# Kernel optimization log

Measured on AMD Instinct MI355X. Metric: run time of the kernel, lower is better.

Reference implementation:

```python
import jax, jax.numpy as jnp
import numpy as np

EMBED, NH, NKV, HD, FF, EPS = 2048, 16, 4, 128, 5632, 1e-5
B, S = 2, 2048

def rmsnorm(x, w):
    xf = x.astype(jnp.float32)
    n = xf * jax.lax.rsqrt(jnp.mean(xf * xf, axis=-1, keepdims=True) + EPS)
    return n.astype(x.dtype) * w

def apply_rope(x, freqs_cis):
    # x: (b, s, h, d); freqs_cis: (s, d//2, 2)
    b, s, h, d = x.shape
    xr = x.astype(jnp.float32).reshape(b, s, h, d // 2, 2)
    f = freqs_cis.reshape(1, s, 1, d // 2, 2)
    out = jnp.stack([xr[..., 0] * f[..., 0] - xr[..., 1] * f[..., 1],
                     xr[..., 1] * f[..., 0] + xr[..., 0] * f[..., 1]], axis=-1)
    return out.reshape(b, s, h, d).astype(x.dtype)

def setup_inputs() -> dict:
    key = jax.random.key(0)
    ks = jax.random.split(key, 8)
    x = jax.random.normal(ks[0], (B, S, EMBED), dtype=jnp.float32)
    attention_mask = jnp.tril(jnp.ones((S, S), dtype=jnp.int32))[None].repeat(B, axis=0)
    # RoPE cos/sin table
    inv = 1.0 / (10000.0 ** (np.arange(0, HD, 2, dtype=np.float32) / HD))
    t = np.arange(S, dtype=np.float32)[:, None] * inv[None, :]  # (S, HD//2)
    freqs_cis = jnp.asarray(np.stack([np.cos(t), np.sin(t)], axis=-1))  # (S, HD//2, 2)
    input_pos = jnp.arange(S, dtype=jnp.int32)
    sd = 0.02
    w_qkv = jax.random.normal(ks[1], ((NH + 2 * NKV) * HD, EMBED), dtype=jnp.float32) * sd
    w_fc = jax.random.normal(ks[2], (EMBED, EMBED), dtype=jnp.float32) * sd
    w1 = jax.random.normal(ks[3], (FF, EMBED), dtype=jnp.float32) * sd
    w2 = jax.random.normal(ks[4], (FF, EMBED), dtype=jnp.float32) * sd
    w3 = jax.random.normal(ks[5], (EMBED, FF), dtype=jnp.float32) * sd
    attn_norm_w = jnp.ones((EMBED,), dtype=jnp.float32)
    ff_norm_w = jnp.ones((EMBED,), dtype=jnp.float32)
    return {"x": x, "attention_mask": attention_mask, "freqs_cis": freqs_cis,
            "input_pos": input_pos, "w_qkv": w_qkv, "w_fc": w_fc,
            "w1": w1, "w2": w2, "w3": w3,
            "attn_norm_w": attn_norm_w, "ff_norm_w": ff_norm_w}

def reference(x, attention_mask, freqs_cis, input_pos, w_qkv, w_fc, w1, w2, w3, attn_norm_w, ff_norm_w):
    b, s, _ = x.shape
    n_rep = NH // NKV
    # --- attention block ---
    h = rmsnorm(x, attn_norm_w)
    qkv = h @ w_qkv.T
    q, k, v = jnp.split(qkv, [NH * HD, NH * HD + NKV * HD], axis=-1)
    q = q.reshape(b, s, NH, HD)
    k = k.reshape(b, s, NKV, HD)
    v = v.reshape(b, s, NKV, HD)
    q = apply_rope(q, freqs_cis)
    k = apply_rope(k, freqs_cis)
    q = q.transpose(0, 2, 1, 3)                       # (b, NH, s, d)
    k = jnp.repeat(k.transpose(0, 2, 1, 3), n_rep, axis=1)  # (b, NH, s, d)
    v = jnp.repeat(v.transpose(0, 2, 1, 3), n_rep, axis=1)
    scale = 1.0 / jnp.sqrt(jnp.float32(EMBED))  # NOTE: source scales by sqrt(embedding_dim)
    scores = jnp.einsum('bhqd,bhkd->bhqk', q, k) * scale
    scores = jnp.where(attention_mask[:, None] == 0, -jnp.inf, scores)
    probs = jax.nn.softmax(scores, axis=-1)
    attn = jnp.einsum('bhqk,bhkd->bhqd', probs, v)
    attn = attn.transpose(0, 2, 1, 3).reshape(b, s, EMBED) @ w_fc.T
    h = x + attn
    # --- SwiGLU FFN ---
    g = rmsnorm(h, ff_norm_w)
    ff = (jax.nn.silu(g @ w1.T) * (g @ w2.T)) @ w3.T
    return h + ff
```

## Files before the change

kernel.cpp:

```cpp
#include <hip/hip_runtime.h>
#include <cstdint>
#include <cstddef>

typedef unsigned short u16;
typedef short bf16x8 __attribute__((ext_vector_type(8)));
typedef float f32x4 __attribute__((ext_vector_type(4)));

#define AS1C(p) ((const __attribute__((address_space(1))) void*)(p))
#define AS3(p)  ((__attribute__((address_space(3))) void*)(p))
#define MFMA_BF16 __builtin_amdgcn_mfma_f32_16x16x32_bf16

__device__ __forceinline__ u16 f2bf(float f) {
    union { float f; unsigned int u; } v; v.f = f;
    unsigned int r = v.u + 0x7fffu + ((v.u >> 16) & 1u);
    return (u16)(r >> 16);
}

struct U16x4 { u16 x, y, z, w; };

__global__ __launch_bounds__(256) void cvt_kernel(const float* __restrict__ src,
                                                  u16* __restrict__ dst, int n4) {
    int i = blockIdx.x * 256 + threadIdx.x;
    if (i < n4) {
        const float4 v = ((const float4*)src)[i];
        U16x4 o; o.x = f2bf(v.x); o.y = f2bf(v.y); o.z = f2bf(v.z); o.w = f2bf(v.w);
        ((U16x4*)dst)[i] = o;
    }
}

__global__ __launch_bounds__(256) void rmsnorm_kernel(const float* __restrict__ X,
                                                      const float* __restrict__ W,
                                                      u16* __restrict__ Out) {
    const int row = blockIdx.x;
    const int t = threadIdx.x;
    const float* xr = X + (size_t)row * 2048;
    float4 a = ((const float4*)xr)[2 * t];
    float4 b = ((const float4*)xr)[2 * t + 1];
    float ss = a.x*a.x + a.y*a.y + a.z*a.z + a.w*a.w
             + b.x*b.x + b.y*b.y + b.z*b.z + b.w*b.w;
    #pragma unroll
    for (int off = 1; off < 64; off <<= 1) ss += __shfl_xor(ss, off);
    __shared__ float red[4];
    if ((t & 63) == 0) red[t >> 6] = ss;
    __syncthreads();
    float tot = red[0] + red[1] + red[2] + red[3];
    float rs = rsqrtf(tot * (1.0f / 2048.0f) + 1e-5f);
    float vals[8] = {a.x, a.y, a.z, a.w, b.x, b.y, b.z, b.w};
    const int base = t * 8;
    u16* orow = Out + (size_t)row * 2048 + base;
    #pragma unroll
    for (int j = 0; j < 8; ++j) orow[j] = f2bf(vals[j] * rs * W[base + j]);
}

__global__ __launch_bounds__(256) void rope_kernel(const float* __restrict__ qkv,
                                                   const float* __restrict__ fr,
                                                   u16* __restrict__ Qo, u16* __restrict__ Ko,
                                                   u16* __restrict__ Vo) {
    const int tok = blockIdx.x;
    const int b = tok >> 11, s = tok & 2047;
    const int t = threadIdx.x;
    const float* row = qkv + (size_t)tok * 3072;
    const float* f = fr + (size_t)s * 128;
    #pragma unroll
    for (int i = 0; i < 4; ++i) {
        int p = t + i * 256;
        int h = p >> 6, pi = p & 63;
        float x0 = row[h * 128 + pi * 2];
        float x1 = row[h * 128 + pi * 2 + 1];
        float c = f[pi * 2], sn = f[pi * 2 + 1];
        size_t ob = ((size_t)(b * 16 + h) * 2048 + s) * 128 + pi * 2;
        Qo[ob]     = f2bf(x0 * c - x1 * sn);
        Qo[ob + 1] = f2bf(x1 * c + x0 * sn);
    }
    {
        int kh = t >> 6, pi = t & 63;
        float x0 = row[2048 + kh * 128 + pi * 2];
        float x1 = row[2048 + kh * 128 + pi * 2 + 1];
        float c = f[pi * 2], sn = f[pi * 2 + 1];
        size_t ob = ((size_t)(b * 4 + kh) * 2048 + s) * 128 + pi * 2;
        Ko[ob]     = f2bf(x0 * c - x1 * sn);
        Ko[ob + 1] = f2bf(x1 * c + x0 * sn);
    }
    #pragma unroll
    for (int i = 0; i < 2; ++i) {
        int e = t + i * 256;
        int kh = e >> 7, d = e & 127;
        Vo[((size_t)(b * 4 + kh) * 128 + d) * 2048 + s] = f2bf(row[2560 + e]);
    }
}

template <bool RESID, bool DUAL>
__global__ __launch_bounds__(256, 2) void gemm_bt(
    const u16* __restrict__ A, const u16* __restrict__ B0, const u16* __restrict__ B1,
    const float* __restrict__ RES, float* __restrict__ Cf, u16* __restrict__ Cb,
    int M, int N, int K) {
    __shared__ __align__(16) u16 As[128 * 32];
    __shared__ __align__(16) u16 Bs[128 * 32];
    __shared__ __align__(16) u16 Bs2[128 * 32];
    const int w = threadIdx.x >> 6;
    const int lane = threadIdx.x & 63;
    const int bm = blockIdx.y * 128;
    const int bn = blockIdx.x * 128;
    const int wm = (w >> 1) * 64;
    const int wn = (w & 1) * 64;
    const int lr = lane & 15;
    const int kq = (lane >> 4) * 8;
    const int srow = lane >> 2;
    const int skc = (lane & 3) * 8;
    f32x4 acc[4][4];
    f32x4 acc2[4][4];
    const f32x4 z = {0.f, 0.f, 0.f, 0.f};
    #pragma unroll
    for (int i = 0; i < 4; ++i)
        #pragma unroll
        for (int j = 0; j < 4; ++j) { acc[i][j] = z; acc2[i][j] = z; }

    for (int k0 = 0; k0 < K; k0 += 32) {
        #pragma unroll
        for (int c = 0; c < 2; ++c) {
            const int chunk = 2 * w + c;
            const int r = chunk * 16 + srow;
            const int lofs = chunk * 512 + lane * 8;
            __builtin_amdgcn_global_load_lds(AS1C(A + (size_t)(bm + r) * K + k0 + skc),
                                             AS3(&As[lofs]), 16, 0, 0);
            __builtin_amdgcn_global_load_lds(AS1C(B0 + (size_t)(bn + r) * K + k0 + skc),
                                             AS3(&Bs[lofs]), 16, 0, 0);
            if constexpr (DUAL)
                __builtin_amdgcn_global_load_lds(AS1C(B1 + (size_t)(bn + r) * K + k0 + skc),
                                                 AS3(&Bs2[lofs]), 16, 0, 0);
        }
        __syncthreads();
        bf16x8 af[4], bfr[4];
        #pragma unroll
        for (int tm = 0; tm < 4; ++tm) af[tm] = *(const bf16x8*)&As[(wm + tm * 16 + lr) * 32 + kq];
        #pragma unroll
        for (int tn = 0; tn < 4; ++tn) bfr[tn] = *(const bf16x8*)&Bs[(wn + tn * 16 + lr) * 32 + kq];
        #pragma unroll
        for (int tm = 0; tm < 4; ++tm)
            #pragma unroll
            for (int tn = 0; tn < 4; ++tn)
                acc[tm][tn] = MFMA_BF16(af[tm], bfr[tn], acc[tm][tn], 0, 0, 0);
        if constexpr (DUAL) {
            #pragma unroll
            for (int tn = 0; tn < 4; ++tn) bfr[tn] = *(const bf16x8*)&Bs2[(wn + tn * 16 + lr) * 32 + kq];
            #pragma unroll
            for (int tm = 0; tm < 4; ++tm)
                #pragma unroll
                for (int tn = 0; tn < 4; ++tn)
                    acc2[tm][tn] = MFMA_BF16(af[tm], bfr[tn], acc2[tm][tn], 0, 0, 0);
        }
        __syncthreads();
    }
    #pragma unroll
    for (int tm = 0; tm < 4; ++tm) {
        const int row0 = bm + wm + tm * 16 + (lane >> 4) * 4;
        #pragma unroll
        for (int tn = 0; tn < 4; ++tn) {
            const int col = bn + wn + tn * 16 + (lane & 15);
            #pragma unroll
            for (int r = 0; r < 4; ++r) {
                const size_t idx = (size_t)(row0 + r) * N + col;
                if constexpr (DUAL) {
                    float aa = acc[tm][tn][r];
                    float bb = acc2[tm][tn][r];
                    float sg = aa / (1.0f + __expf(-aa));
                    Cb[idx] = f2bf(sg * bb);
                } else {
                    float v = acc[tm][tn][r];
                    if constexpr (RESID) v += RES[idx];
                    Cf[idx] = v;
                }
            }
        }
    }
}

__global__ __launch_bounds__(256, 2) void attn_kernel(
    const u16* __restrict__ Q, const u16* __restrict__ Kg,
    const u16* __restrict__ Vt, u16* __restrict__ O) {
    __shared__ __align__(16) u16 Ks[16 * 512];
    __shared__ __align__(16) u16 Vs[16 * 512];
    __shared__ __align__(16) u16 Ps[4][32 * 72];
    const int qt = (int)gridDim.x - 1 - (int)blockIdx.x;
    const int h = blockIdx.y, b = blockIdx.z;
    const int kvh = h >> 2;
    const int w = threadIdx.x >> 6, lane = threadIdx.x & 63;
    const int lr = lane & 15, quad = lane >> 4;
    const int q0 = qt * 128;
    const int wq = q0 + w * 32;
    const u16* kgbase = Kg + (size_t)(b * 4 + kvh) * 2048 * 128;
    const u16* vgbase = Vt + (size_t)(b * 4 + kvh) * 128 * 2048;
    bf16x8 qf[2][4];
    #pragma unroll
    for (int mt = 0; mt < 2; ++mt)
        #pragma unroll
        for (int kk = 0; kk < 4; ++kk)
            qf[mt][kk] = *(const bf16x8*)(Q + ((size_t)(b * 16 + h) * 2048 + wq + mt * 16 + lr) * 128
                                          + kk * 32 + quad * 8);
    f32x4 o[2][8];
    const f32x4 z = {0.f, 0.f, 0.f, 0.f};
    #pragma unroll
    for (int mt = 0; mt < 2; ++mt)
        #pragma unroll
        for (int dt = 0; dt < 8; ++dt) o[mt][dt] = z;
    float m_r[2][4], l_r[2][4];
    #pragma unroll
    for (int mt = 0; mt < 2; ++mt)
        #pragma unroll
        for (int r = 0; r < 4; ++r) { m_r[mt][r] = -1e30f; l_r[mt][r] = 0.f; }
    const float scale = 0.022097086912079608f;
    const float LOG2E = 1.4426950408889634f;
    const int nkt = (q0 + 128) >> 6;

    for (int kt = 0; kt < nkt; ++kt) {
        __syncthreads();
        #pragma unroll
        for (int c = 0; c < 4; ++c) {
            const int i = w * 4 + c;
            __builtin_amdgcn_global_load_lds(
                AS1C(kgbase + (size_t)(kt * 64 + lane) * 128 + i * 8),
                AS3(&Ks[i * 512 + lane * 8]), 16, 0, 0);
            __builtin_amdgcn_global_load_lds(
                AS1C(vgbase + (size_t)((i & 1) * 64 + lane) * 2048 + kt * 64 + (i >> 1) * 8),
                AS3(&Vs[i * 512 + lane * 8]), 16, 0, 0);
        }
        __syncthreads();
        if (kt * 64 <= wq + 31) {
            f32x4 s[2][4];
            #pragma unroll
            for (int mt = 0; mt < 2; ++mt)
                #pragma unroll
                for (int nt = 0; nt < 4; ++nt) s[mt][nt] = z;
            #pragma unroll
            for (int kk = 0; kk < 4; ++kk) {
                bf16x8 kf[4];
                #pragma unroll
                for (int nt = 0; nt < 4; ++nt)
                    kf[nt] = *(const bf16x8*)&Ks[(kk * 4 + quad) * 512 + (nt * 16 + lr) * 8];
                #pragma unroll
                for (int mt = 0; mt < 2; ++mt)
                    #pragma unroll
                    for (int nt = 0; nt < 4; ++nt)
                        s[mt][nt] = MFMA_BF16(qf[mt][kk], kf[nt], s[mt][nt], 0, 0, 0);
            }
            u16* pw = &Ps[w][0];
            #pragma unroll
            for (int mt = 0; mt < 2; ++mt) {
                float mx[4];
                #pragma unroll
                for (int r = 0; r < 4; ++r) {
                    const int rg = wq + mt * 16 + quad * 4 + r;
                    float mm = -1e30f;
                    #pragma unroll
                    for (int nt = 0; nt < 4; ++nt) {
                        const int cg = kt * 64 + nt * 16 + lr;
                        float v = s[mt][nt][r] * scale;
                        if (cg > rg) v = -1e30f;
                        s[mt][nt][r] = v;
                        mm = fmaxf(mm, v);
                    }
                    mx[r] = mm;
                }
                #pragma unroll
                for (int off = 1; off < 16; off <<= 1)
                    #pragma unroll
                    for (int r = 0; r < 4; ++r) mx[r] = fmaxf(mx[r], __shfl_xor(mx[r], off));
                float rsum[4];
                #pragma unroll
                for (int r = 0; r < 4; ++r) {
                    const float mn = fmaxf(m_r[mt][r], mx[r]);
                    const float alpha = exp2f((m_r[mt][r] - mn) * LOG2E);
                    m_r[mt][r] = mn;
                    float rs = 0.f;
                    #pragma unroll
                    for (int nt = 0; nt < 4; ++nt) {
                        float p = exp2f((s[mt][nt][r] - mn) * LOG2E);
                        s[mt][nt][r] = p;
                        rs += p;
                    }
                    rsum[r] = rs;
                    l_r[mt][r] *= alpha;
                    #pragma unroll
                    for (int dt = 0; dt < 8; ++dt) o[mt][dt][r] *= alpha;
                }
                #pragma unroll
                for (int off = 1; off < 16; off <<= 1)
                    #pragma unroll
                    for (int r = 0; r < 4; ++r) rsum[r] += __shfl_xor(rsum[r], off);
                #pragma unroll
                for (int r = 0; r < 4; ++r) l_r[mt][r] += rsum[r];
                #pragma unroll
                for (int nt = 0; nt < 4; ++nt)
                    #pragma unroll
                    for (int r = 0; r < 4; ++r)
                        pw[(mt * 16 + quad * 4 + r) * 72 + nt * 16 + lr] = f2bf(s[mt][nt][r]);
            }
            #pragma unroll
            for (int kf = 0; kf < 2; ++kf) {
                bf16x8 pf[2];
                #pragma unroll
                for (int mt = 0; mt < 2; ++mt)
                    pf[mt] = *(const bf16x8*)&pw[(mt * 16 + lr) * 72 + kf * 32 + quad * 8];
                #pragma unroll
                for (int dt = 0; dt < 8; ++dt) {
                    bf16x8 vf = *(const bf16x8*)&Vs[((kf * 4 + quad) * 2 + (dt >> 2)) * 512
                                                    + ((dt & 3) * 16 + lr) * 8];
                    #pragma unroll
                    for (int mt = 0; mt < 2; ++mt)
                        o[mt][dt] = MFMA_BF16(pf[mt], vf, o[mt][dt], 0, 0, 0);
                }
            }
        }
    }
    #pragma unroll
    for (int mt = 0; mt < 2; ++mt) {
        float inv[4];
        #pragma unroll
        for (int r = 0; r < 4; ++r) inv[r] = 1.0f / l_r[mt][r];
        #pragma unroll
        for (int dt = 0; dt < 8; ++dt)
            #pragma unroll
            for (int r = 0; r < 4; ++r) {
                const int rg = wq + mt * 16 + quad * 4 + r;
                const size_t idx = ((size_t)b * 2048 + rg) * 2048 + h * 128 + dt * 16 + lr;
                O[idx] = f2bf(o[mt][dt][r] * inv[r]);
            }
    }
}

extern "C" void kernel_launch(void* const* d_in, const int* in_sizes, int n_in,
                              void* d_out, int out_size, void* d_ws, size_t ws_size,
                              hipStream_t stream) {
    (void)in_sizes; (void)n_in; (void)out_size; (void)ws_size;
    const float* x    = (const float*)d_in[0];
    const float* fr   = (const float*)d_in[2];
    const float* wqkv = (const float*)d_in[4];
    const float* wfc  = (const float*)d_in[5];
    const float* w1   = (const float*)d_in[6];
    const float* w2   = (const float*)d_in[7];
    const float* w3   = (const float*)d_in[8];
    const float* anw  = (const float*)d_in[9];
    const float* fnw  = (const float*)d_in[10];
    float* out = (float*)d_out;
    char* ws = (char*)d_ws;
    size_t off = 0;
    auto alloc = [&](size_t bytes) -> void* {
        void* p = ws + off;
        off += (bytes + 255) & ~(size_t)255;
        return p;
    };
    u16*   wqkv_b = (u16*)alloc((size_t)3072 * 2048 * 2);
    u16*   wfc_b  = (u16*)alloc((size_t)2048 * 2048 * 2);
    u16*   w1_b   = (u16*)alloc((size_t)5632 * 2048 * 2);
    u16*   w2_b   = (u16*)alloc((size_t)5632 * 2048 * 2);
    u16*   w3_b   = (u16*)alloc((size_t)2048 * 5632 * 2);
    u16*   xn_b   = (u16*)alloc((size_t)4096 * 2048 * 2);
    float* qkv_f  = (float*)alloc((size_t)4096 * 3072 * 4);
    u16*   q_b    = (u16*)alloc((size_t)4096 * 2048 * 2);
    u16*   k_b    = (u16*)alloc((size_t)4096 * 512 * 2);
    u16*   vt_b   = (u16*)alloc((size_t)4096 * 512 * 2);
    float* h_f    = (float*)alloc((size_t)4096 * 2048 * 4);
    u16* attn_b = xn_b;
    u16* t_b    = (u16*)qkv_f;
    u16* g_b    = q_b;

    cvt_kernel<<<6144, 256, 0, stream>>>(wqkv, wqkv_b, 3072 * 2048 / 4);
    cvt_kernel<<<4096, 256, 0, stream>>>(wfc, wfc_b, 2048 * 2048 / 4);
    cvt_kernel<<<11264, 256, 0, stream>>>(w1, w1_b, 5632 * 2048 / 4);
    cvt_kernel<<<11264, 256, 0, stream>>>(w2, w2_b, 5632 * 2048 / 4);
    cvt_kernel<<<11264, 256, 0, stream>>>(w3, w3_b, 2048 * 5632 / 4);

    rmsnorm_kernel<<<4096, 256, 0, stream>>>(x, anw, xn_b);
    gemm_bt<false, false><<<dim3(24, 32), 256, 0, stream>>>(
        xn_b, wqkv_b, nullptr, nullptr, qkv_f, nullptr, 4096, 3072, 2048);
    rope_kernel<<<4096, 256, 0, stream>>>(qkv_f, fr, q_b, k_b, vt_b);
    attn_kernel<<<dim3(16, 16, 2), 256, 0, stream>>>(q_b, k_b, vt_b, attn_b);
    gemm_bt<true, false><<<dim3(16, 32), 256, 0, stream>>>(
        attn_b, wfc_b, nullptr, x, h_f, nullptr, 4096, 2048, 2048);
    rmsnorm_kernel<<<4096, 256, 0, stream>>>(h_f, fnw, g_b);
    gemm_bt<false, true><<<dim3(44, 32), 256, 0, stream>>>(
        g_b, w1_b, w2_b, nullptr, nullptr, t_b, 4096, 5632, 2048);
    gemm_bt<true, false><<<dim3(16, 32), 256, 0, stream>>>(
        t_b, w3_b, nullptr, h_f, out, nullptr, 4096, 2048, 5632);
}
```

Before: 933.6 us.

## Deepen GEMM K-tile with XOR-swizzled LDS, bf16 QKV output, single weight-convert launch

The GEMM now stages 64-wide K slices instead of 32, with an XOR swizzle on the LDS layout to avoid bank conflicts, which halves the barrier count per K. The QKV projection writes bf16 instead of fp32, and the RoPE kernel reads bf16, cutting that intermediate's traffic. The five weight-conversion launches are merged into one kernel over a contiguous buffer. The extra LDS per block (larger for the dual GEMM) may reduce occupancy, and rounding QKV to bf16 before RoPE adds a little precision loss.

```diff
diff --git a/kernel.cpp b/kernel.cpp
--- a/kernel.cpp
+++ b/kernel.cpp
@@ -15,17 +15,28 @@
     unsigned int r = v.u + 0x7fffu + ((v.u >> 16) & 1u);
     return (u16)(r >> 16);
 }
+__device__ __forceinline__ float bf2f(u16 u) {
+    union { unsigned int i; float f; } v; v.i = ((unsigned int)u) << 16; return v.f;
+}
 
 struct U16x4 { u16 x, y, z, w; };
 
-__global__ __launch_bounds__(256) void cvt_kernel(const float* __restrict__ src,
-                                                  u16* __restrict__ dst, int n4) {
-    int i = blockIdx.x * 256 + threadIdx.x;
-    if (i < n4) {
-        const float4 v = ((const float4*)src)[i];
-        U16x4 o; o.x = f2bf(v.x); o.y = f2bf(v.y); o.z = f2bf(v.z); o.w = f2bf(v.w);
-        ((U16x4*)dst)[i] = o;
-    }
+__global__ __launch_bounds__(256) void cvt_all(const float* __restrict__ s0,
+                                               const float* __restrict__ s1,
+                                               const float* __restrict__ s2,
+                                               const float* __restrict__ s3,
+                                               const float* __restrict__ s4,
+                                               u16* __restrict__ dst) {
+    const size_t i = (size_t)blockIdx.x * 256 + threadIdx.x;
+    const float* src; size_t base;
+    if      (i < 1572864u) { src = s0; base = 0; }
+    else if (i < 2621440u) { src = s1; base = 1572864u; }
+    else if (i < 5505024u) { src = s2; base = 2621440u; }
+    else if (i < 8388608u) { src = s3; base = 5505024u; }
+    else                   { src = s4; base = 8388608u; }
+    const float4 v = ((const float4*)src)[i - base];
+    U16x4 o; o.x = f2bf(v.x); o.y = f2bf(v.y); o.z = f2bf(v.z); o.w = f2bf(v.w);
+    ((U16x4*)dst)[i] = o;
 }
 
 __global__ __launch_bounds__(256) void rmsnorm_kernel(const float* __restrict__ X,
@@ -52,21 +63,21 @@
     for (int j = 0; j < 8; ++j) orow[j] = f2bf(vals[j] * rs * W[base + j]);
 }
 
-__global__ __launch_bounds__(256) void rope_kernel(const float* __restrict__ qkv,
+__global__ __launch_bounds__(256) void rope_kernel(const u16* __restrict__ qkv,
                                                    const float* __restrict__ fr,
                                                    u16* __restrict__ Qo, u16* __restrict__ Ko,
                                                    u16* __restrict__ Vo) {
     const int tok = blockIdx.x;
     const int b = tok >> 11, s = tok & 2047;
     const int t = threadIdx.x;
-    const float* row = qkv + (size_t)tok * 3072;
+    const u16* row = qkv + (size_t)tok * 3072;
     const float* f = fr + (size_t)s * 128;
     #pragma unroll
     for (int i = 0; i < 4; ++i) {
         int p = t + i * 256;
         int h = p >> 6, pi = p & 63;
-        float x0 = row[h * 128 + pi * 2];
-        float x1 = row[h * 128 + pi * 2 + 1];
+        float x0 = bf2f(row[h * 128 + pi * 2]);
+        float x1 = bf2f(row[h * 128 + pi * 2 + 1]);
         float c = f[pi * 2], sn = f[pi * 2 + 1];
         size_t ob = ((size_t)(b * 16 + h) * 2048 + s) * 128 + pi * 2;
         Qo[ob]     = f2bf(x0 * c - x1 * sn);
@@ -74,8 +85,8 @@
     }
     {
         int kh = t >> 6, pi = t & 63;
-        float x0 = row[2048 + kh * 128 + pi * 2];
-        float x1 = row[2048 + kh * 128 + pi * 2 + 1];
+        float x0 = bf2f(row[2048 + kh * 128 + pi * 2]);
+        float x1 = bf2f(row[2048 + kh * 128 + pi * 2 + 1]);
         float c = f[pi * 2], sn = f[pi * 2 + 1];
         size_t ob = ((size_t)(b * 4 + kh) * 2048 + s) * 128 + pi * 2;
         Ko[ob]     = f2bf(x0 * c - x1 * sn);
@@ -85,18 +96,18 @@
     for (int i = 0; i < 2; ++i) {
         int e = t + i * 256;
         int kh = e >> 7, d = e & 127;
-        Vo[((size_t)(b * 4 + kh) * 128 + d) * 2048 + s] = f2bf(row[2560 + e]);
-    }
-}
-
-template <bool RESID, bool DUAL>
+        Vo[((size_t)(b * 4 + kh) * 128 + d) * 2048 + s] = row[2560 + e];
+    }
+}
+
+template <bool RESID, bool DUAL, bool BF16OUT>
 __global__ __launch_bounds__(256, 2) void gemm_bt(
     const u16* __restrict__ A, const u16* __restrict__ B0, const u16* __restrict__ B1,
     const float* __restrict__ RES, float* __restrict__ Cf, u16* __restrict__ Cb,
     int M, int N, int K) {
-    __shared__ __align__(16) u16 As[128 * 32];
-    __shared__ __align__(16) u16 Bs[128 * 32];
-    __shared__ __align__(16) u16 Bs2[128 * 32];
+    __shared__ __align__(16) u16 As[128 * 64];
+    __shared__ __align__(16) u16 Bs[128 * 64];
+    __shared__ __align__(16) u16 Bs2[DUAL ? 128 * 64 : 8];
     const int w = threadIdx.x >> 6;
     const int lane = threadIdx.x & 63;
     const int bm = blockIdx.y * 128;
@@ -104,50 +115,65 @@
     const int wm = (w >> 1) * 64;
     const int wn = (w & 1) * 64;
     const int lr = lane & 15;
-    const int kq = (lane >> 4) * 8;
-    const int srow = lane >> 2;
-    const int skc = (lane & 3) * 8;
+    const int quad = lane >> 4;
+    const int srow = lane >> 3;
+    const int sgc = ((lane & 7) ^ (srow & 7)) << 3;
+    const int xq = lr & 7;
     f32x4 acc[4][4];
-    f32x4 acc2[4][4];
+    f32x4 acc2[DUAL ? 4 : 1][DUAL ? 4 : 1];
     const f32x4 z = {0.f, 0.f, 0.f, 0.f};
     #pragma unroll
     for (int i = 0; i < 4; ++i)
         #pragma unroll
-        for (int j = 0; j < 4; ++j) { acc[i][j] = z; acc2[i][j] = z; }
-
-    for (int k0 = 0; k0 < K; k0 += 32) {
-        #pragma unroll
-        for (int c = 0; c < 2; ++c) {
-            const int chunk = 2 * w + c;
-            const int r = chunk * 16 + srow;
-            const int lofs = chunk * 512 + lane * 8;
-            __builtin_amdgcn_global_load_lds(AS1C(A + (size_t)(bm + r) * K + k0 + skc),
+        for (int j = 0; j < 4; ++j) acc[i][j] = z;
+    if constexpr (DUAL) {
+        #pragma unroll
+        for (int i = 0; i < 4; ++i)
+            #pragma unroll
+            for (int j = 0; j < 4; ++j) acc2[i][j] = z;
+    }
+
+    for (int k0 = 0; k0 < K; k0 += 64) {
+        #pragma unroll
+        for (int c = 0; c < 4; ++c) {
+            const int i = w * 4 + c;
+            const int lofs = i * 512 + lane * 8;
+            const int grow = i * 8 + srow;
+            const size_t gofs = (size_t)grow * K + k0 + sgc;
+            __builtin_amdgcn_global_load_lds(AS1C(A + (size_t)bm * K + gofs),
                                              AS3(&As[lofs]), 16, 0, 0);
-            __builtin_amdgcn_global_load_lds(AS1C(B0 + (size_t)(bn + r) * K + k0 + skc),
+            __builtin_amdgcn_global_load_lds(AS1C(B0 + (size_t)bn * K + gofs),
                                              AS3(&Bs[lofs]), 16, 0, 0);
             if constexpr (DUAL)
-                __builtin_amdgcn_global_load_lds(AS1C(B1 + (size_t)(bn + r) * K + k0 + skc),
+                __builtin_amdgcn_global_load_lds(AS1C(B1 + (size_t)bn * K + gofs),
                                                  AS3(&Bs2[lofs]), 16, 0, 0);
         }
         __syncthreads();
-        bf16x8 af[4], bfr[4];
-        #pragma unroll
-        for (int tm = 0; tm < 4; ++tm) af[tm] = *(const bf16x8*)&As[(wm + tm * 16 + lr) * 32 + kq];
-        #pragma unroll
-        for (int tn = 0; tn < 4; ++tn) bfr[tn] = *(const bf16x8*)&Bs[(wn + tn * 16 + lr) * 32 + kq];
-        #pragma unroll
-        for (int tm = 0; tm < 4; ++tm)
+        #pragma unroll
+        for (int kh = 0; kh < 2; ++kh) {
+            const int slot = (((kh << 2) + quad) ^ xq) << 3;
+            bf16x8 af[4], bfr[4];
+            #pragma unroll
+            for (int tm = 0; tm < 4; ++tm)
+                af[tm] = *(const bf16x8*)&As[(wm + tm * 16 + lr) * 64 + slot];
             #pragma unroll
             for (int tn = 0; tn < 4; ++tn)
-                acc[tm][tn] = MFMA_BF16(af[tm], bfr[tn], acc[tm][tn], 0, 0, 0);
-        if constexpr (DUAL) {
-            #pragma unroll
-            for (int tn = 0; tn < 4; ++tn) bfr[tn] = *(const bf16x8*)&Bs2[(wn + tn * 16 + lr) * 32 + kq];
+                bfr[tn] = *(const bf16x8*)&Bs[(wn + tn * 16 + lr) * 64 + slot];
             #pragma unroll
             for (int tm = 0; tm < 4; ++tm)
                 #pragma unroll
                 for (int tn = 0; tn < 4; ++tn)
-                    acc2[tm][tn] = MFMA_BF16(af[tm], bfr[tn], acc2[tm][tn], 0, 0, 0);
+                    acc[tm][tn] = MFMA_BF16(af[tm], bfr[tn], acc[tm][tn], 0, 0, 0);
+            if constexpr (DUAL) {
+                #pragma unroll
+                for (int tn = 0; tn < 4; ++tn)
+                    bfr[tn] = *(const bf16x8*)&Bs2[(wn + tn * 16 + lr) * 64 + slot];
+                #pragma unroll
+                for (int tm = 0; tm < 4; ++tm)
+                    #pragma unroll
+                    for (int tn = 0; tn < 4; ++tn)
+                        acc2[tm][tn] = MFMA_BF16(af[tm], bfr[tn], acc2[tm][tn], 0, 0, 0);
+            }
         }
         __syncthreads();
     }
@@ -165,6 +191,8 @@
                     float bb = acc2[tm][tn][r];
                     float sg = aa / (1.0f + __expf(-aa));
                     Cb[idx] = f2bf(sg * bb);
+                } else if constexpr (BF16OUT) {
+                    Cb[idx] = f2bf(acc[tm][tn][r]);
                 } else {
                     float v = acc[tm][tn][r];
                     if constexpr (RESID) v += RES[idx];
@@ -355,31 +383,27 @@
     u16*   w2_b   = (u16*)alloc((size_t)5632 * 2048 * 2);
     u16*   w3_b   = (u16*)alloc((size_t)2048 * 5632 * 2);
     u16*   xn_b   = (u16*)alloc((size_t)4096 * 2048 * 2);
-    float* qkv_f  = (float*)alloc((size_t)4096 * 3072 * 4);
+    u16*   t_b    = (u16*)alloc((size_t)4096 * 5632 * 2);
     u16*   q_b    = (u16*)alloc((size_t)4096 * 2048 * 2);
     u16*   k_b    = (u16*)alloc((size_t)4096 * 512 * 2);
     u16*   vt_b   = (u16*)alloc((size_t)4096 * 512 * 2);
     float* h_f    = (float*)alloc((size_t)4096 * 2048 * 4);
     u16* attn_b = xn_b;
-    u16* t_b    = (u16*)qkv_f;
+    u16* qkv_b  = t_b;
     u16* g_b    = q_b;
 
-    cvt_kernel<<<6144, 256, 0, stream>>>(wqkv, wqkv_b, 3072 * 2048 / 4);
-    cvt_kernel<<<4096, 256, 0, stream>>>(wfc, wfc_b, 2048 * 2048 / 4);
-    cvt_kernel<<<11264, 256, 0, stream>>>(w1, w1_b, 5632 * 2048 / 4);
-    cvt_kernel<<<11264, 256, 0, stream>>>(w2, w2_b, 5632 * 2048 / 4);
-    cvt_kernel<<<11264, 256, 0, stream>>>(w3, w3_b, 2048 * 5632 / 4);
+    cvt_all<<<44032, 256, 0, stream>>>(wqkv, wfc, w1, w2, w3, wqkv_b);
 
     rmsnorm_kernel<<<4096, 256, 0, stream>>>(x, anw, xn_b);
-    gemm_bt<false, false><<<dim3(24, 32), 256, 0, stream>>>(
-        xn_b, wqkv_b, nullptr, nullptr, qkv_f, nullptr, 4096, 3072, 2048);
-    rope_kernel<<<4096, 256, 0, stream>>>(qkv_f, fr, q_b, k_b, vt_b);
+    gemm_bt<false, false, true><<<dim3(24, 32), 256, 0, stream>>>(
+        xn_b, wqkv_b, nullptr, nullptr, nullptr, qkv_b, 4096, 3072, 2048);
+    rope_kernel<<<4096, 256, 0, stream>>>(qkv_b, fr, q_b, k_b, vt_b);
     attn_kernel<<<dim3(16, 16, 2), 256, 0, stream>>>(q_b, k_b, vt_b, attn_b);
-    gemm_bt<true, false><<<dim3(16, 32), 256, 0, stream>>>(
+    gemm_bt<true, false, false><<<dim3(16, 32), 256, 0, stream>>>(
         attn_b, wfc_b, nullptr, x, h_f, nullptr, 4096, 2048, 2048);
     rmsnorm_kernel<<<4096, 256, 0, stream>>>(h_f, fnw, g_b);
-    gemm_bt<false, true><<<dim3(44, 32), 256, 0, stream>>>(
+    gemm_bt<false, true, true><<<dim3(44, 32), 256, 0, stream>>>(
         g_b, w1_b, w2_b, nullptr, nullptr, t_b, 4096, 5632, 2048);
-    gemm_bt<true, false><<<dim3(16, 32), 256, 0, stream>>>(
+    gemm_bt<true, false, false><<<dim3(16, 32), 256, 0, stream>>>(
         t_b, w3_b, nullptr, h_f, out, nullptr, 4096, 2048, 5632);
 }
```

Measured after the change: 854.8 us. 1.09x faster.
